# Kernel optimization log

Hardware: AMD Instinct MI355X
Metric: run time of the kernel (lower is better)

Reference implementation:

```python
import jax, jax.numpy as jnp
import numpy as np
from jax.scipy.special import erf

B, T, D, H = 256, 128, 128, 1024  # batch, seq_len, enc_in, hid_dim
SIGMA = 0.5  # stochastic-gate sigma (STG FeatureSelector)


def _uniform(key, shape, std):
    return jax.random.uniform(key, shape, jnp.float32, -std, std)


def setup_inputs() -> dict:
    key = jax.random.key(0)
    ks = jax.random.split(key, 16)
    std = 1.0 / np.sqrt(H)
    inp = {
        "x": jax.random.normal(ks[0], (B, T, D), jnp.float32),
        # s_lstm
        "s_x2h_w": _uniform(ks[1], (4 * H, D), std),
        "s_x2h_b": _uniform(ks[2], (4 * H,), std),
        "s_h2h_w": _uniform(ks[3], (4 * H, H), std),
        "s_h2h_b": _uniform(ks[4], (4 * H,), std),
        # p_lstm
        "p_x2h_w": _uniform(ks[5], (4 * H, D), std),
        "p_x2h_b": _uniform(ks[6], (4 * H,), std),
        "p_h2h_w": _uniform(ks[7], (4 * H, H), std),
        "p_h2h_b": _uniform(ks[8], (4 * H,), std),
        # p_fc: hid -> 2*enc_in
        "p_fc_w": _uniform(ks[9], (2 * D, H), std),
        "p_fc_b": _uniform(ks[10], (2 * D,), std),
        # FeatureSelector mu layer: hid -> enc_in
        "fs_w": _uniform(ks[11], (D, H), std),
        "fs_b": _uniform(ks[12], (D,), std),
    }
    return inp


def _lstm_cell(x, h, c, wx, bx, wh, bh):
    gates = x @ wx.T + bx + h @ wh.T + bh          # [B, 4H]
    i, f, g, o = jnp.split(gates, 4, axis=1)
    cy = c * jax.nn.sigmoid(f) + jax.nn.sigmoid(i) * jnp.tanh(g)
    hy = jax.nn.sigmoid(o) * jnp.tanh(cy)
    return hy, cy


def _forward(x, s_x2h_w, s_x2h_b, s_h2h_w, s_h2h_b,
             p_x2h_w, p_x2h_b, p_h2h_w, p_h2h_b,
             p_fc_w, p_fc_b, fs_w, fs_b):
    b = x.shape[0]
    xt = jnp.swapaxes(x, 0, 1)  # [T, B, D] time-major
    sqrt2 = jnp.sqrt(jnp.float32(2.0))

    def step(carry, xs):
        hn, cn, hn2, cn2, mask_prev, xhat0_prev = carry
        x_t, x_tp1 = xs
        # at seq==0 mask_prev=1, xhat0_prev=0 -> input is exactly x_t
        inp = mask_prev * x_t + (1.0 - mask_prev) * xhat0_prev
        hn, cn = _lstm_cell(inp, hn, cn, s_x2h_w, s_x2h_b, s_h2h_w, s_h2h_b)
        # FeatureSelector (eval: noise = 0)
        mu = hn @ fs_w.T + fs_b                     # [B, D]
        z = mu
        mask = jnp.clip(z + 0.5, 0.0, 1.0)          # hard sigmoid gate
        reg = 0.5 * (1.0 + erf((mu + 0.5) / (SIGMA * sqrt2)))  # Phi((mu+0.5)/sigma)
        hn2, cn2 = _lstm_cell(mask * x_tp1, hn2, cn2, p_x2h_w, p_x2h_b, p_h2h_w, p_h2h_b)
        xhat = (hn2 @ p_fc_w.T + p_fc_b).reshape(b, 2, D)
        xhat0, xhat1 = xhat[:, 0, :], xhat[:, 1, :]
        mu_det = jax.lax.stop_gradient(mu)          # torch.tensor(numpy) detaches
        prob_det = jax.lax.stop_gradient(reg)
        outs = (mask, xhat0, xhat1, reg, mu_det, prob_det, z)
        return (hn, cn, hn2, cn2, mask, xhat0), outs

    h0 = jnp.zeros((b, H), x.dtype)
    carry0 = (h0, h0, h0, h0, jnp.ones((b, D), x.dtype), jnp.zeros((b, D), x.dtype))
    _, outs = jax.lax.scan(step, carry0, (xt[:-1], xt[1:]))
    # each out: [T-1, B, D] -> [B, T-1, D]
    return tuple(jnp.swapaxes(o, 0, 1) for o in outs)


def reference(x, s_x2h_w, s_x2h_b, s_h2h_w, s_h2h_b,
              p_x2h_w, p_x2h_b, p_h2h_w, p_h2h_b,
              p_fc_w, p_fc_b, fs_w, fs_b):
    return _forward(x, s_x2h_w, s_x2h_b, s_h2h_w, s_h2h_b,
                    p_x2h_w, p_x2h_b, p_h2h_w, p_h2h_b,
                    p_fc_w, p_fc_b, fs_w, fs_b)
```

## Files before the change

### kernel.cpp

```cpp
#include <hip/hip_runtime.h>
#include <math.h>

#define BB 256
#define TT 128
#define DD 128
#define HH 1024
#define G4 4096
#define TOUT 127
#define OSZ (BB * TOUT * DD)
#define NKB 36
#define ACTE (16 * NKB * 512)

typedef __bf16 bf16x8 __attribute__((ext_vector_type(8)));
typedef float f32x4 __attribute__((ext_vector_type(4)));
typedef unsigned short u16;
typedef unsigned int u32;
typedef unsigned long long u64;

#define MFMA16 __builtin_amdgcn_mfma_f32_16x16x32_bf16

__device__ inline u16 f2bf(float f) {
    union { float f; u32 u; } v; v.f = f;
    u32 r = v.u + 0x7FFFu + ((v.u >> 16) & 1u);
    return (u16)(r >> 16);
}
__device__ inline float fsig(float x)  { return __fdividef(1.0f, 1.0f + __expf(-x)); }
__device__ inline float ftanh(float x) { return __fdividef(2.0f, 1.0f + __expf(-2.0f * x)) - 1.0f; }

__device__ __forceinline__ u64 ldc64(const u64* p) {
    return __hip_atomic_load(p, __ATOMIC_RELAXED, __HIP_MEMORY_SCOPE_AGENT);
}
__device__ __forceinline__ bf16x8 ldc128(const u16* p) {
    union { u64 q[2]; bf16x8 v; } u;
    u.q[0] = ldc64((const u64*)p);
    u.q[1] = ldc64((const u64*)p + 1);
    return u.v;
}
__device__ __forceinline__ void stc32(u16* p, u32 v) {
    __hip_atomic_store((u32*)p, v, __ATOMIC_RELAXED, __HIP_MEMORY_SCOPE_AGENT);
}
__device__ __forceinline__ void stcf(float* p, float v) {
    __hip_atomic_store(p, v, __ATOMIC_RELAXED, __HIP_MEMORY_SCOPE_AGENT);
}
__device__ __forceinline__ float ldcf(const float* p) {
    return __hip_atomic_load(p, __ATOMIC_RELAXED, __HIP_MEMORY_SCOPE_AGENT);
}

struct SArgs {
    u16 *acts, *actp;
    const u16 *wS, *wP, *fswb, *pfcb;
    const float *bS, *bP, *fsb, *pfb, *x;
    float *mbuf, *out;
    u32 *bars, *epoch, *flags;
};

__device__ __forceinline__ void gbar(u32* bars, u32* epoch, u32 gen) {
    asm volatile("s_waitcnt vmcnt(0)" ::: "memory");
    __syncthreads();
    if (threadIdx.x == 0)
        __hip_atomic_fetch_add(&bars[(blockIdx.x & 31) << 4], 1u,
                               __ATOMIC_RELAXED, __HIP_MEMORY_SCOPE_AGENT);
    if (blockIdx.x == 0 && threadIdx.x < 32) {
        while (__hip_atomic_load(&bars[threadIdx.x << 4],
                                 __ATOMIC_RELAXED, __HIP_MEMORY_SCOPE_AGENT) < gen * 8u)
            __builtin_amdgcn_s_sleep(1);
        if (threadIdx.x == 0)
            __hip_atomic_store(epoch, gen, __ATOMIC_RELAXED, __HIP_MEMORY_SCOPE_AGENT);
    }
    if (threadIdx.x == 0) {
        while (__hip_atomic_load(epoch, __ATOMIC_RELAXED, __HIP_MEMORY_SCOPE_AGENT) < gen)
            __builtin_amdgcn_s_sleep(1);
    }
    __syncthreads();
}

__device__ __forceinline__ void gates_tail(
    const SArgs& A, f32x4 acc0, f32x4 acc1,
    const u16* xpart, const u16* wb, const float* bias,
    float* cm, u16* hout, int bm, int bn, int w, int lane)
{
#pragma unroll
    for (int kb = 0; kb < 4; ++kb) {
        bf16x8 a0 = ldc128(xpart + (size_t)kb * 512 + lane * 8);
        bf16x8 a1 = ldc128(xpart + (size_t)(36 + kb) * 512 + lane * 8);
        bf16x8 bv = *(const bf16x8*)(wb + ((size_t)(bn * 8 + w) * 36 + kb) * 512 + lane * 8);
        acc0 = MFMA16(a0, bv, acc0, 0, 0, 0);
        acc1 = MFMA16(a1, bv, acc1, 0, 0, 0);
    }
    const int col = lane & 15, row4 = (lane >> 4) << 2, g0 = lane & 3;
    const int n = bn * 128 + w * 16 + col;
    const int j = n >> 2;
    const float bvv = bias[n];
    const int jl = w * 4 + (col >> 2);
#pragma unroll
    for (int mi = 0; mi < 2; ++mi) {
        f32x4 av = mi ? acc1 : acc0;
#pragma unroll
        for (int rr = 0; rr < 4; ++rr) {
            float v = av[rr] + bvv;
            float v1 = __shfl_xor(v, 1), v2 = __shfl_xor(v, 2), v3 = __shfl_xor(v, 3);
            const int m = bm * 32 + mi * 16 + row4 + rr;
            u32 hb = 0;
            if (g0 == 0) {
                const int ml = mi * 16 + row4 + rr;
                float cp = cm[ml * 32 + jl];
                float cy = cp * fsig(v1) + fsig(v) * ftanh(v2);
                float hy = fsig(v3) * ftanh(cy);
                cm[ml * 32 + jl] = cy;
                hb = (u32)f2bf(hy);
            }
            u32 pv = hb | (((u32)__shfl_xor((int)hb, 4)) << 16);
            if ((lane & 7) == 0)
                stc32(&hout[((size_t)(m >> 4) * 36 + (4 + (j >> 5))) * 512 +
                            ((m & 15) + (((j >> 3) & 3) << 4)) * 8 + (j & 7)], pv);
        }
    }
}

template<int TASK>
__device__ __forceinline__ void gphase(
    const SArgs& A, int t, int bid, int tid, int w, int lane,
    const u64* a_rd, u64* a_wr, const u64* pre_src,
    const u16* xpart, const u16* wb, const float* bias,
    float* cm, u16* hout)
{
    const int bm = bid >> 5, bn = bid & 31;
    const bool dotask = (TASK == 1) ? (bid < 16) : (bid < 32);
    const int tau = bid * 8 + w;

    const u16 *tA = nullptr, *tB = nullptr;
    if (dotask) {
        if (TASK == 1) {
            const int mg = tau >> 3, dg = tau & 7;
            tA = A.acts + ((size_t)mg * 36 + 4) * 512 + lane * 8;
            tB = A.fswb + (size_t)(dg * 32) * 512 + lane * 8;
        } else {
            const int mg = tau >> 4, ng = tau & 15;
            tA = A.actp + ((size_t)mg * 36 + 4) * 512 + lane * 8;
            tB = A.pfcb + (size_t)(ng * 32) * 512 + lane * 8;
        }
    }

    f32x4 acc0 = {}, acc1 = {}, tacc = {};
    const bf16x8* Ard = (const bf16x8*)a_rd;
    const u16* bp = wb + ((size_t)(bn * 8 + w) * 36 + 4) * 512 + lane * 8;
    bf16x8 bcur = *(const bf16x8*)bp;

#pragma unroll 1
    for (int g = 0; g < 4; ++g) {
        u64 pr0, pr1, pr2, pr3;
        {
            const int pb = g * 2048 + tid;
            int p;
            p = pb;        pr0 = ldc64(pre_src + ((p >> 12) * 4608 + 512 + (p & 4095)));
            p = pb + 512;  pr1 = ldc64(pre_src + ((p >> 12) * 4608 + 512 + (p & 4095)));
            p = pb + 1024; pr2 = ldc64(pre_src + ((p >> 12) * 4608 + 512 + (p & 4095)));
            p = pb + 1536; pr3 = ldc64(pre_src + ((p >> 12) * 4608 + 512 + (p & 4095)));
        }
#pragma unroll
        for (int i = 0; i < 8; ++i) {
            const int it = g * 8 + i;
            bf16x8 bnx = *(const bf16x8*)(bp + (size_t)((it < 31) ? (it + 1) : it) * 512);
            bf16x8 a0 = Ard[(size_t)it * 64 + lane];
            bf16x8 a1 = Ard[(size_t)(32 + it) * 64 + lane];
            acc0 = MFMA16(a0, bcur, acc0, 0, 0, 0);
            acc1 = MFMA16(a1, bcur, acc1, 0, 0, 0);
            if (dotask) {
                bf16x8 tav = ldc128(tA + (size_t)it * 512);
                bf16x8 tbv = *(const bf16x8*)(tB + (size_t)it * 512);
                tacc = MFMA16(tav, tbv, tacc, 0, 0, 0);
            }
            bcur = bnx;
        }
        {
            const int pb = g * 2048 + tid;
            a_wr[pb] = pr0; a_wr[pb + 512] = pr1;
            a_wr[pb + 1024] = pr2; a_wr[pb + 1536] = pr3;
        }
    }

    if (dotask) {
        const int col = lane & 15, row4 = (lane >> 4) << 2;
        if (TASK == 1) {
            const int mg = tau >> 3, dg = tau & 7;
            const int d = dg * 16 + col;
            const float bv = A.fsb[d];
#pragma unroll
            for (int rr = 0; rr < 4; ++rr) {
                const int m = mg * 16 + row4 + rr;
                float mu = tacc[rr] + bv;
                float mask = fminf(fmaxf(mu + 0.5f, 0.f), 1.f);
                float reg = 0.5f * (1.f + erff((mu + 0.5f) * 1.41421356237f));
                const size_t o = (size_t)m * (TOUT * DD) + (size_t)t * DD + d;
                A.out[o] = mask;
                A.out[o + 3 * (size_t)OSZ] = reg;
                A.out[o + 4 * (size_t)OSZ] = mu;
                A.out[o + 5 * (size_t)OSZ] = reg;
                A.out[o + 6 * (size_t)OSZ] = mu;
                stcf(&A.mbuf[m * DD + d], mask);
                float xv = A.x[(size_t)m * (TT * DD) + (size_t)(t + 1) * DD + d];
                u32 xb = (u32)f2bf(mask * xv);
                u32 pv = xb | (((u32)__shfl_xor((int)xb, 1)) << 16);
                if ((lane & 1) == 0)
                    stc32(&A.actp[((size_t)(m >> 4) * 36 + (d >> 5)) * 512 +
                                  ((m & 15) + (((d >> 3) & 3) << 4)) * 8 + (d & 7)], pv);
            }
        } else {
            const int mg = tau >> 4, ng = tau & 15;
            const int n = ng * 16 + col;
            const float bv = A.pfb[n];
#pragma unroll
            for (int rr = 0; rr < 4; ++rr) {
                const int m = mg * 16 + row4 + rr;
                float v = tacc[rr] + bv;
                const size_t ob = (size_t)m * (TOUT * DD) + (size_t)t * DD;
                if (ng < 8) {
                    A.out[ob + n + (size_t)OSZ] = v;
                    float mk = ldcf(&A.mbuf[m * DD + n]);
                    float xv = A.x[(size_t)m * (TT * DD) + (size_t)(t + 1) * DD + n];
                    u32 ib = (u32)f2bf(mk * xv + (1.f - mk) * v);
                    u32 pv = ib | (((u32)__shfl_xor((int)ib, 1)) << 16);
                    if ((lane & 1) == 0)
                        stc32(&A.acts[((size_t)(m >> 4) * 36 + (n >> 5)) * 512 +
                                      ((m & 15) + (((n >> 3) & 3) << 4)) * 8 + (n & 7)], pv);
                } else {
                    A.out[ob + (n - DD) + 2 * (size_t)OSZ] = v;
                }
            }
        }
        asm volatile("s_waitcnt vmcnt(0)" ::: "memory");
        if (lane == 0) {
            const int f = (TASK == 1) ? tau : (128 + tau);
            __hip_atomic_store(&A.flags[f << 4], (u32)(t + 1),
                               __ATOMIC_RELAXED, __HIP_MEMORY_SCOPE_AGENT);
        }
    }

    if (w == 0 && lane < 16) {
        const int f = (TASK == 1) ? (16 * bm + lane)
                                  : (128 + 32 * bm + (lane & 7) + ((lane >> 3) << 4));
        const u32 need = (u32)(t + 1);
        while (__hip_atomic_load(&A.flags[f << 4],
                                 __ATOMIC_RELAXED, __HIP_MEMORY_SCOPE_AGENT) < need)
            __builtin_amdgcn_s_sleep(1);
    }
    __syncthreads();

    gates_tail(A, acc0, acc1, xpart, wb, bias, cm, hout, bm, bn, w, lane);
}

__global__ __launch_bounds__(512, 1) void k_scan(SArgs A)
{
    __shared__ __align__(16) u64 aS[8192];
    __shared__ __align__(16) u64 aP[8192];
    __shared__ float cst[2][32][32];

    const int bid = blockIdx.x, tid = threadIdx.x;
    const int w = tid >> 6, lane = tid & 63;
    const int bm = bid >> 5;

    for (int i = tid; i < 2 * 32 * 32; i += 512) ((float*)cst)[i] = 0.f;
    for (int i = tid; i < 8192; i += 512) aP[i] = 0;
    __syncthreads();

    u32 gen = 0;

    {
        f32x4 z0 = {}, z1 = {};
        gates_tail(A, z0, z1, A.acts + (size_t)(2 * bm) * 36 * 512, A.wS, A.bS,
                   &cst[0][0][0], A.acts, bm, bid & 31, w, lane);
        gbar(A.bars, A.epoch, ++gen);
    }

    for (int t = 0; t < TOUT; ++t) {
        gphase<1>(A, t, bid, tid, w, lane, aP, aS,
                  (const u64*)A.acts + (size_t)(2 * bm) * 4608,
                  A.actp + (size_t)(2 * bm) * 36 * 512,
                  A.wP, A.bP, &cst[1][0][0], A.actp);
        gbar(A.bars, A.epoch, ++gen);

        if (t < TOUT - 1) {
            gphase<2>(A, t, bid, tid, w, lane, aS, aP,
                      (const u64*)A.actp + (size_t)(2 * bm) * 4608,
                      A.acts + (size_t)(2 * bm) * 36 * 512,
                      A.wS, A.bS, &cst[0][0][0], A.acts);
            gbar(A.bars, A.epoch, ++gen);
        } else {
            if (bid < 32) {
                const int tau = bid * 8 + w;
                const int mg = tau >> 4, ng = tau & 15;
                const u16* tA = A.actp + ((size_t)mg * 36 + 4) * 512 + lane * 8;
                const u16* tB = A.pfcb + (size_t)(ng * 32) * 512 + lane * 8;
                f32x4 tacc = {};
#pragma unroll 8
                for (int it = 0; it < 32; ++it) {
                    bf16x8 tav = ldc128(tA + (size_t)it * 512);
                    bf16x8 tbv = *(const bf16x8*)(tB + (size_t)it * 512);
                    tacc = MFMA16(tav, tbv, tacc, 0, 0, 0);
                }
                const int col = lane & 15, row4 = (lane >> 4) << 2;
                const int n = ng * 16 + col;
                const float bv = A.pfb[n];
#pragma unroll
                for (int rr = 0; rr < 4; ++rr) {
                    const int m = mg * 16 + row4 + rr;
                    float v = tacc[rr] + bv;
                    const size_t ob = (size_t)m * (TOUT * DD) + (size_t)t * DD;
                    if (ng < 8) A.out[ob + n + (size_t)OSZ] = v;
                    else        A.out[ob + (n - DD) + 2 * (size_t)OSZ] = v;
                }
            }
        }
    }
}


__global__ void k_wgates(const float* __restrict__ wx, const float* __restrict__ wh,
                         u16* __restrict__ blob) {
    int i = blockIdx.x * 256 + threadIdx.x;
    if (i >= 256 * NKB * 64) return;
    int lane = i & 63, cblk = (i >> 6) % NKB, rblk = (i >> 6) / NKB;
    int n = (rblk << 4) | (lane & 15);
    int c = (cblk << 5) + ((lane >> 4) << 3);
    int orow = ((n & 3) << 10) | (n >> 2);
    const float* s = (cblk < 4) ? (wx + (size_t)orow * DD + c)
                                : (wh + (size_t)orow * HH + (c - 128));
    u16* d = blob + (size_t)i * 8;
#pragma unroll
    for (int k = 0; k < 8; ++k) d[k] = f2bf(s[k]);
}

__global__ void k_wplain(const float* __restrict__ wsrc, u16* __restrict__ blob,
                         int nblk, int K) {
    int CB = K >> 5;
    int i = blockIdx.x * 256 + threadIdx.x;
    if (i >= nblk * CB * 64) return;
    int lane = i & 63, cblk = (i >> 6) % CB, rblk = (i >> 6) / CB;
    int r = (rblk << 4) | (lane & 15);
    int c = (cblk << 5) + ((lane >> 4) << 3);
    const float* s = wsrc + (size_t)r * K + c;
    u16* d = blob + (size_t)i * 8;
#pragma unroll
    for (int k = 0; k < 8; ++k) d[k] = f2bf(s[k]);
}

__global__ void k_bias2(const float* __restrict__ bx, const float* __restrict__ bh,
                        float* __restrict__ dst) {
    int r = blockIdx.x * 256 + threadIdx.x;
    if (r < G4) {
        int o = ((r & 3) << 10) | (r >> 2);
        dst[r] = bx[o] + bh[o];
    }
}

__global__ void k_zero(u16* acts, u16* actp, float* mbuf,
                       u32* bars, u32* epoch, u32* flags) {
    size_t i = (size_t)blockIdx.x * 256 + threadIdx.x;
    if (i < (size_t)ACTE) { acts[i] = 0; actp[i] = 0; }
    if (i < (size_t)BB * DD) mbuf[i] = 0.f;
    if (i < 512) bars[i] = 0;
    if (i < 16) epoch[i] = 0;
    if (i < 6144) flags[i] = 0;
}

__global__ void k_fillx(const float* __restrict__ x, u16* __restrict__ acts) {
    int i = blockIdx.x * 256 + threadIdx.x;
    if (i >= BB * DD) return;
    int m = i >> 7, d = i & 127;
    acts[(((size_t)(m >> 4) * NKB + (d >> 5)) * 64 +
          ((m & 15) + (((d >> 3) & 3) << 4))) * 8 + (d & 7)] =
        f2bf(x[(size_t)m * (TT * DD) + d]);
}

extern "C" void kernel_launch(void* const* d_in, const int* in_sizes, int n_in,
                              void* d_out, int out_size, void* d_ws, size_t ws_size,
                              hipStream_t stream) {
    const float* x       = (const float*)d_in[0];
    const float* s_x2h_w = (const float*)d_in[1];
    const float* s_x2h_b = (const float*)d_in[2];
    const float* s_h2h_w = (const float*)d_in[3];
    const float* s_h2h_b = (const float*)d_in[4];
    const float* p_x2h_w = (const float*)d_in[5];
    const float* p_x2h_b = (const float*)d_in[6];
    const float* p_h2h_w = (const float*)d_in[7];
    const float* p_h2h_b = (const float*)d_in[8];
    const float* p_fc_w  = (const float*)d_in[9];
    const float* p_fc_b  = (const float*)d_in[10];
    const float* fs_w    = (const float*)d_in[11];
    const float* fs_b    = (const float*)d_in[12];

    char* ws = (char*)d_ws;
    size_t off = 0;
    auto alloc = [&](size_t bytes) { void* p = ws + off; off += (bytes + 255) & ~(size_t)255; return p; };
    u16*   wS    = (u16*)  alloc((size_t)G4 * 1152 * 2);
    u16*   wP    = (u16*)  alloc((size_t)G4 * 1152 * 2);
    u16*   fswb  = (u16*)  alloc((size_t)8 * 32 * 512 * 2);
    u16*   pfcb  = (u16*)  alloc((size_t)16 * 32 * 512 * 2);
    float* bS    = (float*)alloc((size_t)G4 * 4);
    float* bP    = (float*)alloc((size_t)G4 * 4);
    u16*   acts  = (u16*)  alloc((size_t)ACTE * 2);
    u16*   actp  = (u16*)  alloc((size_t)ACTE * 2);
    float* mbuf  = (float*)alloc((size_t)BB * DD * 4);
    u32*   bars  = (u32*)  alloc(512 * 4);
    u32*   epoch = (u32*)  alloc(16 * 4);
    u32*   flags = (u32*)  alloc(6144 * 4);

    k_wgates<<<dim3(2304), 256, 0, stream>>>(s_x2h_w, s_h2h_w, wS);
    k_wgates<<<dim3(2304), 256, 0, stream>>>(p_x2h_w, p_h2h_w, wP);
    k_wplain<<<dim3(64),  256, 0, stream>>>(fs_w, fswb, 8, 1024);
    k_wplain<<<dim3(128), 256, 0, stream>>>(p_fc_w, pfcb, 16, 1024);
    k_bias2<<<dim3(16), 256, 0, stream>>>(s_x2h_b, s_h2h_b, bS);
    k_bias2<<<dim3(16), 256, 0, stream>>>(p_x2h_b, p_h2h_b, bP);
    k_zero<<<dim3(1152), 256, 0, stream>>>(acts, actp, mbuf, bars, epoch, flags);
    k_fillx<<<dim3(128), 256, 0, stream>>>(x, acts);

    SArgs sa;
    sa.acts = acts; sa.actp = actp;
    sa.wS = wS; sa.wP = wP; sa.fswb = fswb; sa.pfcb = pfcb;
    sa.bS = bS; sa.bP = bP; sa.fsb = fs_b; sa.pfb = p_fc_b; sa.x = x;
    sa.mbuf = mbuf; sa.out = (float*)d_out;
    sa.bars = bars; sa.epoch = epoch; sa.flags = flags;

    void* kargs[] = { &sa };
    hipError_t e = hipLaunchCooperativeKernel((const void*)k_scan, dim3(256), dim3(512),
                                              kargs, 0, stream);
    if (e != hipSuccess) {
        k_scan<<<dim3(256), dim3(512), 0, stream>>>(sa);
    }
}
```

Baseline: 5.509 ms.

## Replace grid barriers with per-row-group flag dataflow and double-buffered activations

Removes the global grid barrier between LSTM phases. Each block now publishes progress flags and waits only on the 32 blocks in its batch row group that produce its inputs. The activation buffers for both LSTMs are double-buffered by time-step parity so that later steps cannot overwrite data still being read. The small FC and feature-selector tasks are redistributed to warp 7 of every block instead of a few whole blocks. The intent is to cut barrier latency and let row groups drift apart, at the cost of twice the activation memory and more complex flag ordering.

```diff
diff --git a/kernel.cpp b/kernel.cpp
--- a/kernel.cpp
+++ b/kernel.cpp
@@ -45,37 +45,24 @@
 __device__ __forceinline__ float ldcf(const float* p) {
     return __hip_atomic_load(p, __ATOMIC_RELAXED, __HIP_MEMORY_SCOPE_AGENT);
 }
+__device__ __forceinline__ void fpoll(const u32* f, int idx, u32 need) {
+    while (__hip_atomic_load(&f[idx << 4], __ATOMIC_RELAXED, __HIP_MEMORY_SCOPE_AGENT) < need)
+        __builtin_amdgcn_s_sleep(1);
+}
+__device__ __forceinline__ void fpub(u32* f, int idx, u32 v) {
+    __hip_atomic_store(&f[idx << 4], v, __ATOMIC_RELAXED, __HIP_MEMORY_SCOPE_AGENT);
+}
 
 struct SArgs {
-    u16 *acts, *actp;
+    u16 *acts0, *acts1, *actp0, *actp1;
     const u16 *wS, *wP, *fswb, *pfcb;
     const float *bS, *bP, *fsb, *pfb, *x;
     float *mbuf, *out;
-    u32 *bars, *epoch, *flags;
+    u32 *fS, *fP, *fM, *fF;
 };
 
-__device__ __forceinline__ void gbar(u32* bars, u32* epoch, u32 gen) {
-    asm volatile("s_waitcnt vmcnt(0)" ::: "memory");
-    __syncthreads();
-    if (threadIdx.x == 0)
-        __hip_atomic_fetch_add(&bars[(blockIdx.x & 31) << 4], 1u,
-                               __ATOMIC_RELAXED, __HIP_MEMORY_SCOPE_AGENT);
-    if (blockIdx.x == 0 && threadIdx.x < 32) {
-        while (__hip_atomic_load(&bars[threadIdx.x << 4],
-                                 __ATOMIC_RELAXED, __HIP_MEMORY_SCOPE_AGENT) < gen * 8u)
-            __builtin_amdgcn_s_sleep(1);
-        if (threadIdx.x == 0)
-            __hip_atomic_store(epoch, gen, __ATOMIC_RELAXED, __HIP_MEMORY_SCOPE_AGENT);
-    }
-    if (threadIdx.x == 0) {
-        while (__hip_atomic_load(epoch, __ATOMIC_RELAXED, __HIP_MEMORY_SCOPE_AGENT) < gen)
-            __builtin_amdgcn_s_sleep(1);
-    }
-    __syncthreads();
-}
-
 __device__ __forceinline__ void gates_tail(
-    const SArgs& A, f32x4 acc0, f32x4 acc1,
+    f32x4 acc0, f32x4 acc1,
     const u16* xpart, const u16* wb, const float* bias,
     float* cm, u16* hout, int bm, int bn, int w, int lane)
 {
@@ -121,22 +108,23 @@
 __device__ __forceinline__ void gphase(
     const SArgs& A, int t, int bid, int tid, int w, int lane,
     const u64* a_rd, u64* a_wr, const u64* pre_src,
+    const u16* tAbase, u16* xinDst,
     const u16* xpart, const u16* wb, const float* bias,
     float* cm, u16* hout)
 {
     const int bm = bid >> 5, bn = bid & 31;
-    const bool dotask = (TASK == 1) ? (bid < 16) : (bid < 32);
-    const int tau = bid * 8 + w;
+    const bool dotask = (TASK == 1) ? (w == 7 && bn < 16) : (w == 7);
+    const int tau = (TASK == 1) ? (bm * 16 + bn) : (bm * 32 + bn);
 
     const u16 *tA = nullptr, *tB = nullptr;
     if (dotask) {
         if (TASK == 1) {
             const int mg = tau >> 3, dg = tau & 7;
-            tA = A.acts + ((size_t)mg * 36 + 4) * 512 + lane * 8;
+            tA = tAbase + ((size_t)mg * 36 + 4) * 512 + lane * 8;
             tB = A.fswb + (size_t)(dg * 32) * 512 + lane * 8;
         } else {
             const int mg = tau >> 4, ng = tau & 15;
-            tA = A.actp + ((size_t)mg * 36 + 4) * 512 + lane * 8;
+            tA = tAbase + ((size_t)mg * 36 + 4) * 512 + lane * 8;
             tB = A.pfcb + (size_t)(ng * 32) * 512 + lane * 8;
         }
     }
@@ -202,7 +190,7 @@
                 u32 xb = (u32)f2bf(mask * xv);
                 u32 pv = xb | (((u32)__shfl_xor((int)xb, 1)) << 16);
                 if ((lane & 1) == 0)
-                    stc32(&A.actp[((size_t)(m >> 4) * 36 + (d >> 5)) * 512 +
+                    stc32(&xinDst[((size_t)(m >> 4) * 36 + (d >> 5)) * 512 +
                                   ((m & 15) + (((d >> 3) & 3) << 4)) * 8 + (d & 7)], pv);
             }
         } else {
@@ -221,7 +209,7 @@
                     u32 ib = (u32)f2bf(mk * xv + (1.f - mk) * v);
                     u32 pv = ib | (((u32)__shfl_xor((int)ib, 1)) << 16);
                     if ((lane & 1) == 0)
-                        stc32(&A.acts[((size_t)(m >> 4) * 36 + (n >> 5)) * 512 +
+                        stc32(&xinDst[((size_t)(m >> 4) * 36 + (n >> 5)) * 512 +
                                       ((m & 15) + (((n >> 3) & 3) << 4)) * 8 + (n & 7)], pv);
                 } else {
                     A.out[ob + (n - DD) + 2 * (size_t)OSZ] = v;
@@ -229,24 +217,17 @@
             }
         }
         asm volatile("s_waitcnt vmcnt(0)" ::: "memory");
-        if (lane == 0) {
-            const int f = (TASK == 1) ? tau : (128 + tau);
-            __hip_atomic_store(&A.flags[f << 4], (u32)(t + 1),
-                               __ATOMIC_RELAXED, __HIP_MEMORY_SCOPE_AGENT);
-        }
+        if (lane == 0)
+            fpub((TASK == 1) ? A.fM : A.fF, tau, (u32)(t + 1));
     }
 
     if (w == 0 && lane < 16) {
-        const int f = (TASK == 1) ? (16 * bm + lane)
-                                  : (128 + 32 * bm + (lane & 7) + ((lane >> 3) << 4));
-        const u32 need = (u32)(t + 1);
-        while (__hip_atomic_load(&A.flags[f << 4],
-                                 __ATOMIC_RELAXED, __HIP_MEMORY_SCOPE_AGENT) < need)
-            __builtin_amdgcn_s_sleep(1);
+        if (TASK == 1) fpoll(A.fM, bm * 16 + lane, (u32)(t + 1));
+        else           fpoll(A.fF, bm * 32 + (lane & 7) + ((lane >> 3) << 4), (u32)(t + 1));
     }
     __syncthreads();
 
-    gates_tail(A, acc0, acc1, xpart, wb, bias, cm, hout, bm, bn, w, lane);
+    gates_tail(acc0, acc1, xpart, wb, bias, cm, hout, bm, bn, w, lane);
 }
 
 __global__ __launch_bounds__(512, 1) void k_scan(SArgs A)
@@ -257,60 +238,48 @@
 
     const int bid = blockIdx.x, tid = threadIdx.x;
     const int w = tid >> 6, lane = tid & 63;
-    const int bm = bid >> 5;
+    const int bm = bid >> 5, bn = bid & 31;
 
     for (int i = tid; i < 2 * 32 * 32; i += 512) ((float*)cst)[i] = 0.f;
     for (int i = tid; i < 8192; i += 512) aP[i] = 0;
     __syncthreads();
 
-    u32 gen = 0;
-
     {
         f32x4 z0 = {}, z1 = {};
-        gates_tail(A, z0, z1, A.acts + (size_t)(2 * bm) * 36 * 512, A.wS, A.bS,
-                   &cst[0][0][0], A.acts, bm, bid & 31, w, lane);
-        gbar(A.bars, A.epoch, ++gen);
+        gates_tail(z0, z1, A.acts0 + (size_t)(2 * bm) * 36 * 512, A.wS, A.bS,
+                   &cst[0][0][0], A.acts0, bm, bn, w, lane);
+        asm volatile("s_waitcnt vmcnt(0)" ::: "memory");
+        __syncthreads();
+        if (tid == 0) fpub(A.fS, bid, 1u);
     }
 
     for (int t = 0; t < TOUT; ++t) {
+        const int par = t & 1;
+        u16* hsb = par ? A.acts1 : A.acts0;
+        u16* hpb = par ? A.actp1 : A.actp0;
+        u16* nsb = par ? A.acts0 : A.acts1;
+
+        if (w == 0 && lane < 32) fpoll(A.fS, bm * 32 + lane, (u32)(t + 1));
+        __syncthreads();
         gphase<1>(A, t, bid, tid, w, lane, aP, aS,
-                  (const u64*)A.acts + (size_t)(2 * bm) * 4608,
-                  A.actp + (size_t)(2 * bm) * 36 * 512,
-                  A.wP, A.bP, &cst[1][0][0], A.actp);
-        gbar(A.bars, A.epoch, ++gen);
-
-        if (t < TOUT - 1) {
-            gphase<2>(A, t, bid, tid, w, lane, aS, aP,
-                      (const u64*)A.actp + (size_t)(2 * bm) * 4608,
-                      A.acts + (size_t)(2 * bm) * 36 * 512,
-                      A.wS, A.bS, &cst[0][0][0], A.acts);
-            gbar(A.bars, A.epoch, ++gen);
-        } else {
-            if (bid < 32) {
-                const int tau = bid * 8 + w;
-                const int mg = tau >> 4, ng = tau & 15;
-                const u16* tA = A.actp + ((size_t)mg * 36 + 4) * 512 + lane * 8;
-                const u16* tB = A.pfcb + (size_t)(ng * 32) * 512 + lane * 8;
-                f32x4 tacc = {};
-#pragma unroll 8
-                for (int it = 0; it < 32; ++it) {
-                    bf16x8 tav = ldc128(tA + (size_t)it * 512);
-                    bf16x8 tbv = *(const bf16x8*)(tB + (size_t)it * 512);
-                    tacc = MFMA16(tav, tbv, tacc, 0, 0, 0);
-                }
-                const int col = lane & 15, row4 = (lane >> 4) << 2;
-                const int n = ng * 16 + col;
-                const float bv = A.pfb[n];
-#pragma unroll
-                for (int rr = 0; rr < 4; ++rr) {
-                    const int m = mg * 16 + row4 + rr;
-                    float v = tacc[rr] + bv;
-                    const size_t ob = (size_t)m * (TOUT * DD) + (size_t)t * DD;
-                    if (ng < 8) A.out[ob + n + (size_t)OSZ] = v;
-                    else        A.out[ob + (n - DD) + 2 * (size_t)OSZ] = v;
-                }
-            }
-        }
+                  (const u64*)hsb + (size_t)(2 * bm) * 4608,
+                  hsb, hpb,
+                  hpb + (size_t)(2 * bm) * 36 * 512,
+                  A.wP, A.bP, &cst[1][0][0], hpb);
+        asm volatile("s_waitcnt vmcnt(0)" ::: "memory");
+        __syncthreads();
+        if (tid == 0) fpub(A.fP, bid, (u32)(t + 1));
+
+        if (w == 0 && lane < 32) fpoll(A.fP, bm * 32 + lane, (u32)(t + 1));
+        __syncthreads();
+        gphase<2>(A, t, bid, tid, w, lane, aS, aP,
+                  (const u64*)hpb + (size_t)(2 * bm) * 4608,
+                  hpb, nsb,
+                  nsb + (size_t)(2 * bm) * 36 * 512,
+                  A.wS, A.bS, &cst[0][0][0], nsb);
+        asm volatile("s_waitcnt vmcnt(0)" ::: "memory");
+        __syncthreads();
+        if (tid == 0) fpub(A.fS, bid, (u32)(t + 2));
     }
 }
 
@@ -353,14 +322,11 @@
     }
 }
 
-__global__ void k_zero(u16* acts, u16* actp, float* mbuf,
-                       u32* bars, u32* epoch, u32* flags) {
+__global__ void k_zero(u16* acts, u16* actp, float* mbuf, u32* flags) {
     size_t i = (size_t)blockIdx.x * 256 + threadIdx.x;
-    if (i < (size_t)ACTE) { acts[i] = 0; actp[i] = 0; }
+    if (i < 2 * (size_t)ACTE) { acts[i] = 0; actp[i] = 0; }
     if (i < (size_t)BB * DD) mbuf[i] = 0.f;
-    if (i < 512) bars[i] = 0;
-    if (i < 16) epoch[i] = 0;
-    if (i < 6144) flags[i] = 0;
+    if (i < 14336) flags[i] = 0;
 }
 
 __global__ void k_fillx(const float* __restrict__ x, u16* __restrict__ acts) {
@@ -398,12 +364,10 @@
     u16*   pfcb  = (u16*)  alloc((size_t)16 * 32 * 512 * 2);
     float* bS    = (float*)alloc((size_t)G4 * 4);
     float* bP    = (float*)alloc((size_t)G4 * 4);
-    u16*   acts  = (u16*)  alloc((size_t)ACTE * 2);
-    u16*   actp  = (u16*)  alloc((size_t)ACTE * 2);
+    u16*   acts  = (u16*)  alloc((size_t)2 * ACTE * 2);
+    u16*   actp  = (u16*)  alloc((size_t)2 * ACTE * 2);
     float* mbuf  = (float*)alloc((size_t)BB * DD * 4);
-    u32*   bars  = (u32*)  alloc(512 * 4);
-    u32*   epoch = (u32*)  alloc(16 * 4);
-    u32*   flags = (u32*)  alloc(6144 * 4);
+    u32*   flags = (u32*)  alloc(14336 * 4);
 
     k_wgates<<<dim3(2304), 256, 0, stream>>>(s_x2h_w, s_h2h_w, wS);
     k_wgates<<<dim3(2304), 256, 0, stream>>>(p_x2h_w, p_h2h_w, wP);
@@ -411,15 +375,19 @@
     k_wplain<<<dim3(128), 256, 0, stream>>>(p_fc_w, pfcb, 16, 1024);
     k_bias2<<<dim3(16), 256, 0, stream>>>(s_x2h_b, s_h2h_b, bS);
     k_bias2<<<dim3(16), 256, 0, stream>>>(p_x2h_b, p_h2h_b, bP);
-    k_zero<<<dim3(1152), 256, 0, stream>>>(acts, actp, mbuf, bars, epoch, flags);
+    k_zero<<<dim3(2304), 256, 0, stream>>>(acts, actp, mbuf, flags);
     k_fillx<<<dim3(128), 256, 0, stream>>>(x, acts);
 
     SArgs sa;
-    sa.acts = acts; sa.actp = actp;
+    sa.acts0 = acts; sa.acts1 = acts + ACTE;
+    sa.actp0 = actp; sa.actp1 = actp + ACTE;
     sa.wS = wS; sa.wP = wP; sa.fswb = fswb; sa.pfcb = pfcb;
     sa.bS = bS; sa.bP = bP; sa.fsb = fs_b; sa.pfb = p_fc_b; sa.x = x;
     sa.mbuf = mbuf; sa.out = (float*)d_out;
-    sa.bars = bars; sa.epoch = epoch; sa.flags = flags;
+    sa.fS = flags;
+    sa.fP = flags + 4096;
+    sa.fM = flags + 8192;
+    sa.fF = flags + 10240;
 
     void* kargs[] = { &sa };
     hipError_t e = hipLaunchCooperativeKernel((const void*)k_scan, dim3(256), dim3(512),
```

Result: faster. 5.144 ms (-6.6%).
